# Kernel tuning notes

Hardware: AMD Instinct MI355X
Metric: run time of the kernel (lower is better)

The kernel has to match this reference:

```python
import jax, jax.numpy as jnp
import numpy as np

VOCAB = 32000
D_MODEL = 192
N_LAYERS = 8
D_STATE = 64
EXPAND = 2
D_CONV = 3
NUM_CLASSES = 2
D_INNER = EXPAND * D_MODEL            # 384
DT_RANK = (D_MODEL + 15) // 16        # 12 (mamba_ssm default ceil(d_model/16))
EPS = 1e-6


def rmsnorm(x, w):
    return w * x * jax.lax.rsqrt(jnp.mean(x * x, axis=-1, keepdims=True) + EPS)


def selective_scan(u, dt, A, Bm, Cm):
    # u, dt: (b, T, d_inner); Bm, Cm: (b, T, d_state); A: (d_inner, d_state)
    def step(h, xs):
        dt_t, B_t, C_t, u_t = xs                      # (b,di),(b,ds),(b,ds),(b,di)
        dA = jnp.exp(dt_t[:, :, None] * A)            # (b, di, ds)
        h = dA * h + (dt_t * u_t)[:, :, None] * B_t[:, None, :]
        y = jnp.einsum('bdn,bn->bd', h, C_t)
        return h, y

    b = u.shape[0]
    h0 = jnp.zeros((b, D_INNER, D_STATE), u.dtype)
    xs = (jnp.swapaxes(dt, 0, 1), jnp.swapaxes(Bm, 0, 1),
          jnp.swapaxes(Cm, 0, 1), jnp.swapaxes(u, 0, 1))
    _, ys = jax.lax.scan(step, h0, xs)                # ys: (T, b, di)
    return jnp.swapaxes(ys, 0, 1)


def mamba_layer(x, p):
    # one residual Mamba block: x + Mamba(RMSNorm(x))
    norm_w, in_w, cw, cb, xpw, dtw, dtb, Alog, Dp, ow = p
    h = rmsnorm(x, norm_w)
    xz = jnp.einsum('btd,ed->bte', h, in_w)           # (b, T, 2*di)
    xi, z = jnp.split(xz, 2, axis=-1)
    # causal depthwise conv over time
    xc = jnp.swapaxes(xi, 1, 2)                       # (b, di, T)
    xc = jax.lax.conv_general_dilated(xc, cw[:, None, :], (1,),
                                      [(D_CONV - 1, 0)],
                                      feature_group_count=D_INNER)
    xi = jax.nn.silu(jnp.swapaxes(xc, 1, 2) + cb)
    dbl = jnp.einsum('btc,ec->bte', xi, xpw)          # (b, T, dt_rank+2*ds)
    dt_r = dbl[..., :DT_RANK]
    Bm = dbl[..., DT_RANK:DT_RANK + D_STATE]
    Cm = dbl[..., DT_RANK + D_STATE:]
    dt = jax.nn.softplus(jnp.einsum('btr,dr->btd', dt_r, dtw) + dtb)
    A = -jnp.exp(Alog)
    y = selective_scan(xi, dt, A, Bm, Cm) + xi * Dp
    y = y * jax.nn.silu(z)
    return x + jnp.einsum('bte,de->btd', y, ow)


def setup_inputs():
    key = jax.random.key(0)
    ks = jax.random.split(key, 12)
    B, L = 8, 1024
    s = 0.02
    input_ids = jax.random.randint(ks[0], (B, L), 0, VOCAB, dtype=jnp.int32)
    attention_mask = jnp.ones((B, L), dtype=jnp.int32)
    embed = jax.random.normal(ks[1], (VOCAB, D_MODEL), jnp.float32) * s
    cls = jax.random.normal(ks[2], (1, 1, D_MODEL), jnp.float32) * s
    norm_w = jnp.ones((N_LAYERS, D_MODEL), jnp.float32)
    in_proj_w = jax.random.normal(ks[3], (N_LAYERS, 2 * D_INNER, D_MODEL), jnp.float32) * s
    conv_w = jax.random.normal(ks[4], (N_LAYERS, D_INNER, D_CONV), jnp.float32) * s
    conv_b = jnp.zeros((N_LAYERS, D_INNER), jnp.float32)
    x_proj_w = jax.random.normal(ks[5], (N_LAYERS, DT_RANK + 2 * D_STATE, D_INNER), jnp.float32) * s
    dt_proj_w = jax.random.normal(ks[6], (N_LAYERS, D_INNER, DT_RANK), jnp.float32) * s
    dt_proj_b = jnp.zeros((N_LAYERS, D_INNER), jnp.float32)
    # mamba_ssm S4D-real init: A_log = log(1..d_state)
    A_log = jnp.log(jnp.tile(jnp.arange(1.0, D_STATE + 1, dtype=jnp.float32)[None, None, :],
                             (N_LAYERS, D_INNER, 1)))
    D_param = jnp.ones((N_LAYERS, D_INNER), jnp.float32)
    out_proj_w = jax.random.normal(ks[7], (N_LAYERS, D_MODEL, D_INNER), jnp.float32) * s
    final_norm_w = jnp.ones((D_MODEL,), jnp.float32)
    head_w = embed[:NUM_CLASSES]            # tie_embeddings=True
    head_b = jnp.zeros((NUM_CLASSES,), jnp.float32)
    return dict(input_ids=input_ids, attention_mask=attention_mask, embed=embed,
                cls=cls, norm_w=norm_w, in_proj_w=in_proj_w, conv_w=conv_w,
                conv_b=conv_b, x_proj_w=x_proj_w, dt_proj_w=dt_proj_w,
                dt_proj_b=dt_proj_b, A_log=A_log, D_param=D_param,
                out_proj_w=out_proj_w, final_norm_w=final_norm_w,
                head_w=head_w, head_b=head_b)


def reference(input_ids, attention_mask, embed, cls, norm_w, in_proj_w, conv_w,
              conv_b, x_proj_w, dt_proj_w, dt_proj_b, A_log, D_param,
              out_proj_w, final_norm_w, head_w, head_b):
    x = embed[input_ids]                               # (b, L, d)
    b = x.shape[0]
    x = jnp.concatenate([x, jnp.broadcast_to(cls, (b, 1, D_MODEL))], axis=1)
    layer_fn = jax.checkpoint(mamba_layer)

    def body(x, p):
        return layer_fn(x, p), None

    x, _ = jax.lax.scan(body, x, (norm_w, in_proj_w, conv_w, conv_b, x_proj_w,
                                  dt_proj_w, dt_proj_b, A_log, D_param, out_proj_w))
    x = rmsnorm(x, final_norm_w)
    m = attention_mask.astype(x.dtype)                 # (b, L)
    denom = jnp.clip(jnp.sum(m, axis=1, keepdims=True), 1.0, None)
    pooled = jnp.sum(x[:, :-1] * m[..., None], axis=1) / denom
    return pooled @ head_w.T + head_b                  # (b, num_classes)
```

## Files before the change

### kernel.cpp

```cpp
#include <hip/hip_runtime.h>
#include <hip/hip_bf16.h>
#include <cstddef>

namespace {

constexpr int NB   = 8;
constexpr int LSEQ = 1025;
constexpr int TSEQ = 1024;
constexpr int DM   = 192;
constexpr int DI   = 384;
constexpr int DXZ  = 768;
constexpr int DBLW = 140;
constexpr int DTR  = 12;
constexpr int NST  = 64;
constexpr int MROWS = NB * LSEQ;
constexpr int NCH  = 64;
constexpr int CS   = 16;
constexpr int NCH1 = NCH - 1;
constexpr int NDG  = DI / 64;
constexpr int HST  = 32;
constexpr int XPAD = 144;
constexpr float LOG2E = 1.4426950408889634f;

using bf16x8 = __attribute__((ext_vector_type(8))) short;
using f32x4  = __attribute__((ext_vector_type(4))) float;

__device__ __forceinline__ float waveReduceSum(float v) {
#pragma unroll
  for (int o = 32; o; o >>= 1) v += __shfl_xor(v, o, 64);
  return v;
}

__device__ __forceinline__ unsigned short f2bf(float v) {
  __hip_bfloat16 b = __float2bfloat16(v);
  return *reinterpret_cast<unsigned short*>(&b);
}
__device__ __forceinline__ float bf2f(unsigned short u) {
  return __uint_as_float(((unsigned)u) << 16);
}
__device__ __forceinline__ unsigned addpair_bf(unsigned a, unsigned b) {
  float alo = __uint_as_float(a << 16), ahi = __uint_as_float(a & 0xffff0000u);
  float blo = __uint_as_float(b << 16), bhi = __uint_as_float(b & 0xffff0000u);
  return ((unsigned)f2bf(alo + blo)) | (((unsigned)f2bf(ahi + bhi)) << 16);
}

__global__ void embed_kernel(const int* __restrict__ ids, const float* __restrict__ emb,
                             const float* __restrict__ cls, float* __restrict__ x) {
  int idx = blockIdx.x * blockDim.x + threadIdx.x;
  if (idx >= NB * LSEQ * DM) return;
  int d = idx % DM;
  int bt = idx / DM;
  int t = bt % LSEQ, b = bt / LSEQ;
  float v;
  if (t < TSEQ) v = emb[(size_t)ids[b * TSEQ + t] * DM + d];
  else          v = cls[d];
  x[idx] = v;
}

__global__ void cvt_bf16_kernel(const float* __restrict__ src, unsigned short* __restrict__ dst,
                                int n) {
  int idx = blockIdx.x * blockDim.x + threadIdx.x;
  if (idx < n) dst[idx] = f2bf(src[idx]);
}

__global__ void pad_xp_kernel(const float* __restrict__ src, unsigned short* __restrict__ dst) {
  int idx = blockIdx.x * blockDim.x + threadIdx.x;
  if (idx >= 8 * XPAD * DI) return;
  int k = idx % DI;
  int n = (idx / DI) % XPAD;
  int l = idx / (DI * XPAD);
  float v = (n < DBLW) ? src[((size_t)l * DBLW + n) * DI + k] : 0.f;
  dst[idx] = f2bf(v);
}

__global__ void transpose_batched(const float* __restrict__ in, float* __restrict__ out,
                                  int rows, int cols) {
  __shared__ float tile[32][33];
  int l = blockIdx.z;
  int r0 = blockIdx.y * 32, c0 = blockIdx.x * 32;
  const float* src = in + (size_t)l * rows * cols;
  float* dst = out + (size_t)l * rows * cols;
  int tx = threadIdx.x, ty = threadIdx.y;
#pragma unroll
  for (int i = 0; i < 32; i += 8) {
    int r = r0 + ty + i, c = c0 + tx;
    if (r < rows && c < cols) tile[ty + i][tx] = src[(size_t)r * cols + c];
  }
  __syncthreads();
#pragma unroll
  for (int i = 0; i < 32; i += 8) {
    int c = c0 + ty + i, r = r0 + tx;
    if (c < cols && r < rows) dst[(size_t)c * rows + r] = tile[tx][ty + i];
  }
}

__global__ __launch_bounds__(192)
void rmsnorm_kernel(const float* __restrict__ x, const float* __restrict__ w,
                    unsigned short* __restrict__ h) {
  int row = blockIdx.x;
  int d = threadIdx.x;
  float v = x[(size_t)row * DM + d];
  float ss = waveReduceSum(v * v);
  __shared__ float red[3];
  if ((d & 63) == 0) red[d >> 6] = ss;
  __syncthreads();
  float ms = (red[0] + red[1] + red[2]) * (1.f / DM);
  h[(size_t)row * DM + d] = f2bf(v * rsqrtf(ms + 1e-6f) * w[d]);
}

template <int EPI, int ASRC>
__global__ __launch_bounds__(256)
void gemm_mfma(const unsigned short* __restrict__ A, const unsigned short* __restrict__ Ab0,
               const unsigned short* __restrict__ Ab1, const unsigned short* __restrict__ W,
               float* __restrict__ C, unsigned short* __restrict__ Cb,
               int M, int Nw, int Nstore, int K, int ldc) {
  __shared__ unsigned short Alds[128][40];
  __shared__ unsigned short Wlds[64][40];
  const int tid = threadIdx.x;
  const int w = tid >> 6, lane = tid & 63;
  const int r16 = lane & 15, g = lane >> 4;
  const int row0 = blockIdx.y * 128, col0 = blockIdx.x * 64;

  f32x4 acc[2][4];
#pragma unroll
  for (int mi = 0; mi < 2; ++mi)
#pragma unroll
    for (int ni = 0; ni < 4; ++ni) acc[mi][ni] = (f32x4){0.f, 0.f, 0.f, 0.f};

  for (int k0 = 0; k0 < K; k0 += 32) {
#pragma unroll
    for (int cc = 0; cc < 2; ++cc) {
      int c = tid + cc * 256;
      int r = c >> 2, q = c & 3;
      uint4 v = make_uint4(0, 0, 0, 0);
      int grow = row0 + r;
      if (grow < M) {
        if (ASRC == 0) {
          v = *(const uint4*)(A + (size_t)grow * K + k0 + q * 8);
        } else {
          uint4 a = *(const uint4*)(Ab0 + (size_t)grow * K + k0 + q * 8);
          uint4 b = *(const uint4*)(Ab1 + (size_t)grow * K + k0 + q * 8);
          v.x = addpair_bf(a.x, b.x);
          v.y = addpair_bf(a.y, b.y);
          v.z = addpair_bf(a.z, b.z);
          v.w = addpair_bf(a.w, b.w);
        }
      }
      *(uint4*)&Alds[r][q * 8] = v;
    }
    {
      int r = tid >> 2, q = tid & 3;
      uint4 v = make_uint4(0, 0, 0, 0);
      int gn = col0 + r;
      if (gn < Nw) v = *(const uint4*)(W + (size_t)gn * K + k0 + q * 8);
      *(uint4*)&Wlds[r][q * 8] = v;
    }
    __syncthreads();
    bf16x8 a_f[2], b_f[4];
#pragma unroll
    for (int mi = 0; mi < 2; ++mi)
      a_f[mi] = *(const bf16x8*)&Alds[w * 32 + mi * 16 + r16][g * 8];
#pragma unroll
    for (int ni = 0; ni < 4; ++ni)
      b_f[ni] = *(const bf16x8*)&Wlds[ni * 16 + r16][g * 8];
#pragma unroll
    for (int mi = 0; mi < 2; ++mi)
#pragma unroll
      for (int ni = 0; ni < 4; ++ni)
        acc[mi][ni] = __builtin_amdgcn_mfma_f32_16x16x32_bf16(a_f[mi], b_f[ni],
                                                              acc[mi][ni], 0, 0, 0);
    __syncthreads();
  }
#pragma unroll
  for (int mi = 0; mi < 2; ++mi) {
#pragma unroll
    for (int reg = 0; reg < 4; ++reg) {
      int row = row0 + w * 32 + mi * 16 + g * 4 + reg;
      if (row >= M) continue;
#pragma unroll
      for (int ni = 0; ni < 4; ++ni) {
        int col = col0 + ni * 16 + r16;
        if (col >= Nstore) continue;
        size_t idx = (size_t)row * ldc + col;
        if (EPI == 1)      C[idx] += acc[mi][ni][reg];
        else if (EPI == 0) C[idx] = acc[mi][ni][reg];
        else               Cb[idx] = f2bf(acc[mi][ni][reg]);
      }
    }
  }
}

__global__ void conv_kernel(const unsigned short* __restrict__ xz16, const float* __restrict__ cw,
                            const float* __restrict__ cb,
                            unsigned short* __restrict__ xi16,
                            unsigned short* __restrict__ zg16) {
  int idx = blockIdx.x * blockDim.x + threadIdx.x;
  if (idx >= NB * LSEQ * DI) return;
  int c = idx % DI;
  int bt = idx / DI;
  int t = bt % LSEQ, b = bt / LSEQ;
  const unsigned short* src = xz16 + (size_t)b * LSEQ * DXZ + c;
  float s = cb[c];
  float w0 = cw[c * 3 + 0], w1 = cw[c * 3 + 1], w2 = cw[c * 3 + 2];
  if (t >= 2) s = fmaf(w0, bf2f(src[(size_t)(t - 2) * DXZ]), s);
  if (t >= 1) s = fmaf(w1, bf2f(src[(size_t)(t - 1) * DXZ]), s);
  s = fmaf(w2, bf2f(src[(size_t)t * DXZ]), s);
  float sig = 1.f / (1.f + __expf(-s));
  float u = s * sig;
  xi16[idx] = f2bf(u);
  float zv = bf2f(src[(size_t)t * DXZ + DI]);
  float zsig = 1.f / (1.f + __expf(-zv));
  zg16[idx] = f2bf(zv * zsig);
}

__global__ __launch_bounds__(384)
void dt_kernel(const float* __restrict__ dbl, const float* __restrict__ dtwT,
               const float* __restrict__ dtb, float* __restrict__ dtout) {
  int row0 = blockIdx.x * 4;
  int d = threadIdx.x;
  __shared__ float rr[4][DTR];
  if (d < 4 * DTR) rr[d / DTR][d % DTR] = dbl[(size_t)(row0 + d / DTR) * DBLW + (d % DTR)];
  float w[DTR];
#pragma unroll
  for (int r = 0; r < DTR; ++r) w[r] = dtwT[r * DI + d];
  float bias = dtb[d];
  __syncthreads();
#pragma unroll
  for (int q = 0; q < 4; ++q) {
    float s = bias;
#pragma unroll
    for (int r = 0; r < DTR; ++r) s = fmaf(rr[q][r], w[r], s);
    float sp = fmaxf(s, 0.f) + log1pf(__expf(-fabsf(s)));
    dtout[(size_t)(row0 + q) * DI + d] = sp;
  }
}


__global__ __launch_bounds__(768, 6)
void scan_pass1(const float* __restrict__ dtp_, const unsigned short* __restrict__ xi16,
                const float* __restrict__ dbl, const float* __restrict__ Alog,
                float* __restrict__ cumdt, float* __restrict__ H) {
  __shared__ float Bt[CS][64];
  const int tid = threadIdx.x;
  const int w = tid >> 6, lane = tid & 63;
  const int dgrp = w >> 1, half = w & 1;
  const int b = blockIdx.x / NCH1;
  const int c = blockIdx.x % NCH1;
  const int bg = b * NDG + dgrp;
  const int d = dgrp * 64 + lane;
  const int n0 = half * HST;
  const int t0 = c * CS;

  {
    const float* srcB = dbl + ((size_t)b * LSEQ + t0) * DBLW + DTR + lane;
    for (int r = w; r < CS; r += 12) Bt[r][lane] = srcB[(size_t)r * DBLW];
  }

  const float* Ap = Alog + (size_t)d * NST;
  float a0 = __expf(Ap[0]);
  bool okl = true;
#pragma unroll
  for (int j = 0; j < HST; ++j) {
    float aj = __expf(Ap[n0 + j]);
    okl = okl && (fabsf(aj - (float)(n0 + j + 1) * a0) <= 1e-3f * (float)(n0 + j + 1) * fabsf(a0));
  }
  const bool fast = __all(okl);
  const float al2u = -a0 * LOG2E;

  float h[HST];
#pragma unroll
  for (int j = 0; j < HST; ++j) h[j] = 0.f;

  __syncthreads();

  const float* dtp = dtp_ + ((size_t)b * LSEQ + t0) * DI + d;
  const unsigned short* up = xi16 + ((size_t)b * LSEQ + t0) * DI + d;
  float cum = 0.f;
  float dtv = *dtp, uv = bf2f(*up);

  if (fast) {
    for (int t = 0; t < CS; ++t) {
      float n_dt = 0.f, n_u = 0.f;
      if (t + 1 < CS) {
        dtp += DI; up += DI;
        n_dt = *dtp; n_u = bf2f(*up);
      }
      float dtu = dtv * uv;
      float m = dtv * al2u;
      float r1 = exp2f(m);
      float p = (n0 == 0) ? r1 : exp2f(m * (float)(n0 + 1));
      float r2 = r1 * r1, r4 = r2 * r2;
      float s0 = p, s1 = p * r1, s2 = p * r2, s3 = s2 * r1;
#pragma unroll
      for (int k = 0; k < 8; ++k) {
        float4 B4 = *(const float4*)&Bt[t][n0 + 4 * k];
        h[4 * k + 0] = fmaf(s0, h[4 * k + 0], dtu * B4.x);
        h[4 * k + 1] = fmaf(s1, h[4 * k + 1], dtu * B4.y);
        h[4 * k + 2] = fmaf(s2, h[4 * k + 2], dtu * B4.z);
        h[4 * k + 3] = fmaf(s3, h[4 * k + 3], dtu * B4.w);
        if (k < 7) { s0 *= r4; s1 *= r4; s2 *= r4; s3 *= r4; }
      }
      cum += dtv;
      dtv = n_dt; uv = n_u;
    }
  } else {
    for (int t = 0; t < CS; ++t) {
      float n_dt = 0.f, n_u = 0.f;
      if (t + 1 < CS) {
        dtp += DI; up += DI;
        n_dt = *dtp; n_u = bf2f(*up);
      }
      float dtu = dtv * uv;
      for (int j = 0; j < HST; ++j) {
        float aj = -__expf(Ap[n0 + j]) * LOG2E;
        h[j] = fmaf(exp2f(dtv * aj), h[j], dtu * Bt[t][n0 + j]);
      }
      cum += dtv;
      dtv = n_dt; uv = n_u;
    }
  }

  if (half == 0)
    cumdt[(size_t)bg * NCH1 * 64 + (size_t)c * 64 + lane] = cum;
  float* hp = H + ((size_t)bg * NCH + (c + 1)) * NST * 64 + (size_t)n0 * 64 + lane;
#pragma unroll
  for (int j = 0; j < HST; ++j) hp[j * 64] = h[j];
}

__global__ __launch_bounds__(256)
void scan_pass2(const float* __restrict__ cumdt, const float* __restrict__ Alog,
                float* __restrict__ H) {
  int gw = blockIdx.x * 4 + (threadIdx.x >> 6);
  int lane = threadIdx.x & 63;
  int bg = gw >> 4;
  int nq = (gw & 15) * 4;
  int dgrp = bg % NDG;
  int d = dgrp * 64 + lane;

  float al2[4];
#pragma unroll
  for (int j = 0; j < 4; ++j) al2[j] = -__expf(Alog[(size_t)d * NST + nq + j]) * LOG2E;

  float h[4] = {0.f, 0.f, 0.f, 0.f};

  float* H0 = H + ((size_t)bg * NCH) * NST * 64 + (size_t)nq * 64 + lane;
#pragma unroll
  for (int j = 0; j < 4; ++j) H0[j * 64] = 0.f;

  for (int c = 1; c < NCH; ++c) {
    float cum = cumdt[(size_t)bg * NCH1 * 64 + (size_t)(c - 1) * 64 + lane];
    float* Hc = H + ((size_t)bg * NCH + c) * NST * 64 + (size_t)nq * 64 + lane;
#pragma unroll
    for (int j = 0; j < 4; ++j) {
      float he = Hc[j * 64];
      h[j] = fmaf(exp2f(al2[j] * cum), h[j], he);
      Hc[j * 64] = h[j];
    }
  }
}

__global__ __launch_bounds__(768, 6)
void scan_pass3(const float* __restrict__ dtp_, const unsigned short* __restrict__ xi16,
                const unsigned short* __restrict__ zg16, const float* __restrict__ dbl,
                const float* __restrict__ Alog, const float* __restrict__ Dpar,
                const float* __restrict__ H, unsigned short* __restrict__ yb0,
                unsigned short* __restrict__ yb1) {
  __shared__ float Bt[CS + 1][64];
  __shared__ float Ct[CS + 1][64];
  const int tid = threadIdx.x;
  const int w = tid >> 6, lane = tid & 63;
  const int dgrp = w >> 1, half = w & 1;
  const int b = blockIdx.x >> 6;
  const int c = blockIdx.x & 63;
  const int bg = b * NDG + dgrp;
  const int d = dgrp * 64 + lane;
  const int n0 = half * HST;
  const int t0 = c * CS;
  const int nsteps = (c == NCH - 1) ? (LSEQ - t0) : CS;

  {
    if (w < 6) {
      const float* srcB = dbl + ((size_t)b * LSEQ + t0) * DBLW + DTR + lane;
      for (int r = w; r < nsteps; r += 6) Bt[r][lane] = srcB[(size_t)r * DBLW];
    } else {
      const float* srcC = dbl + ((size_t)b * LSEQ + t0) * DBLW + DTR + NST + lane;
      for (int r = w - 6; r < nsteps; r += 6) Ct[r][lane] = srcC[(size_t)r * DBLW];
    }
  }

  const float* Ap = Alog + (size_t)d * NST;
  float a0 = __expf(Ap[0]);
  bool okl = true;
#pragma unroll
  for (int j = 0; j < HST; ++j) {
    float aj = __expf(Ap[n0 + j]);
    okl = okl && (fabsf(aj - (float)(n0 + j + 1) * a0) <= 1e-3f * (float)(n0 + j + 1) * fabsf(a0));
  }
  const bool fast = __all(okl);
  const float al2u = -a0 * LOG2E;

  float Dp = Dpar[d];
  float h[HST];
  {
    const float* hi = H + ((size_t)bg * NCH + c) * NST * 64 + (size_t)n0 * 64 + lane;
#pragma unroll
    for (int j = 0; j < HST; ++j) h[j] = hi[j * 64];
  }

  __syncthreads();

  const float* dtp = dtp_ + ((size_t)b * LSEQ + t0) * DI + d;
  const unsigned short* up = xi16 + ((size_t)b * LSEQ + t0) * DI + d;
  const unsigned short* gp = zg16 + ((size_t)b * LSEQ + t0) * DI + d;
  unsigned short* yp = (half == 0 ? yb0 : yb1) + ((size_t)b * LSEQ + t0) * DI + d;

  float dtv = *dtp, uv = bf2f(*up), gv = bf2f(*gp);

  if (fast) {
    for (int t = 0; t < nsteps; ++t) {
      float n_dt = 0.f, n_u = 0.f, n_g = 0.f;
      if (t + 1 < nsteps) {
        dtp += DI; up += DI; gp += DI;
        n_dt = *dtp; n_u = bf2f(*up); n_g = bf2f(*gp);
      }
      float dtu = dtv * uv;
      float m = dtv * al2u;
      float r1 = exp2f(m);
      float p = (n0 == 0) ? r1 : exp2f(m * (float)(n0 + 1));
      float r2 = r1 * r1, r4 = r2 * r2;
      float s0 = p, s1 = p * r1, s2 = p * r2, s3 = s2 * r1;
      float y = 0.f;
#pragma unroll
      for (int k = 0; k < 8; ++k) {
        float4 B4 = *(const float4*)&Bt[t][n0 + 4 * k];
        float4 C4 = *(const float4*)&Ct[t][n0 + 4 * k];
        h[4 * k + 0] = fmaf(s0, h[4 * k + 0], dtu * B4.x);
        y = fmaf(h[4 * k + 0], C4.x, y);
        h[4 * k + 1] = fmaf(s1, h[4 * k + 1], dtu * B4.y);
        y = fmaf(h[4 * k + 1], C4.y, y);
        h[4 * k + 2] = fmaf(s2, h[4 * k + 2], dtu * B4.z);
        y = fmaf(h[4 * k + 2], C4.z, y);
        h[4 * k + 3] = fmaf(s3, h[4 * k + 3], dtu * B4.w);
        y = fmaf(h[4 * k + 3], C4.w, y);
        if (k < 7) { s0 *= r4; s1 *= r4; s2 *= r4; s3 *= r4; }
      }
      float outv = (half == 0) ? fmaf(uv, Dp, y) * gv : y * gv;
      *yp = f2bf(outv);
      yp += DI;
      dtv = n_dt; uv = n_u; gv = n_g;
    }
  } else {
    for (int t = 0; t < nsteps; ++t) {
      float n_dt = 0.f, n_u = 0.f, n_g = 0.f;
      if (t + 1 < nsteps) {
        dtp += DI; up += DI; gp += DI;
        n_dt = *dtp; n_u = bf2f(*up); n_g = bf2f(*gp);
      }
      float dtu = dtv * uv;
      float y = 0.f;
      for (int j = 0; j < HST; ++j) {
        float aj = -__expf(Ap[n0 + j]) * LOG2E;
        h[j] = fmaf(exp2f(dtv * aj), h[j], dtu * Bt[t][n0 + j]);
        y = fmaf(h[j], Ct[t][n0 + j], y);
      }
      float outv = (half == 0) ? fmaf(uv, Dp, y) * gv : y * gv;
      *yp = f2bf(outv);
      yp += DI;
      dtv = n_dt; uv = n_u; gv = n_g;
    }
  }
}

__global__ __launch_bounds__(192)
void pool1_kernel(const float* __restrict__ x, const int* __restrict__ mask,
                  const float* __restrict__ fw, float* __restrict__ partial) {
  int b = blockIdx.x >> 6;
  int chunk = blockIdx.x & 63;
  int d = threadIdx.x;
  __shared__ float red[3];
  float w = fw[d];
  float acc = 0.f;
  for (int tt = 0; tt < 16; ++tt) {
    int t = chunk * 16 + tt;
    float v = x[((size_t)b * LSEQ + t) * DM + d];
    float ss = waveReduceSum(v * v);
    if ((d & 63) == 0) red[d >> 6] = ss;
    __syncthreads();
    float ms = (red[0] + red[1] + red[2]) * (1.f / DM);
    float m = (float)mask[b * TSEQ + t];
    acc = fmaf(v * rsqrtf(ms + 1e-6f) * w, m, acc);
    __syncthreads();
  }
  partial[((size_t)b * 64 + chunk) * DM + d] = acc;
}

__global__ __launch_bounds__(192)
void pool2_kernel(const float* __restrict__ partial, const int* __restrict__ mask,
                  const float* __restrict__ hw, const float* __restrict__ hb,
                  float* __restrict__ out) {
  int b = blockIdx.x;
  int d = threadIdx.x;
  float s = 0.f;
  for (int c = 0; c < 64; ++c) s += partial[((size_t)b * 64 + c) * DM + d];
  float den = 0.f;
  for (int t = d; t < TSEQ; t += DM) den += (float)mask[b * TSEQ + t];
  den = waveReduceSum(den);
  __shared__ float dred[3];
  __shared__ float pooled[DM];
  if ((d & 63) == 0) dred[d >> 6] = den;
  __syncthreads();
  float denom = fmaxf(dred[0] + dred[1] + dred[2], 1.f);
  pooled[d] = s / denom;
  __syncthreads();
  if (d < 2) {
    float acc = hb[d];
    for (int k = 0; k < DM; ++k) acc = fmaf(pooled[k], hw[d * DM + k], acc);
    out[b * 2 + d] = acc;
  }
}

}

extern "C" void kernel_launch(void* const* d_in, const int* in_sizes, int n_in,
                              void* d_out, int out_size, void* d_ws, size_t ws_size,
                              hipStream_t stream) {
  const int*   ids    = (const int*)d_in[0];
  const int*   mask   = (const int*)d_in[1];
  const float* embed  = (const float*)d_in[2];
  const float* cls    = (const float*)d_in[3];
  const float* norm_w = (const float*)d_in[4];
  const float* in_w   = (const float*)d_in[5];
  const float* conv_w = (const float*)d_in[6];
  const float* conv_b = (const float*)d_in[7];
  const float* xp_w   = (const float*)d_in[8];
  const float* dtw    = (const float*)d_in[9];
  const float* dtb    = (const float*)d_in[10];
  const float* Alog   = (const float*)d_in[11];
  const float* Dpar   = (const float*)d_in[12];
  const float* ow     = (const float*)d_in[13];
  const float* fnw    = (const float*)d_in[14];
  const float* hw     = (const float*)d_in[15];
  const float* hb     = (const float*)d_in[16];
  float* out = (float*)d_out;

  char* base = (char*)d_ws;
  size_t off = 0;
  auto alloc = [&](size_t bytes) -> void* {
    void* p = base + off;
    off = (off + bytes + 255) & ~(size_t)255;
    return p;
  };

  float* x      = (float*)alloc((size_t)NB * LSEQ * DM * 4);
  unsigned short* h16 = (unsigned short*)alloc((size_t)NB * LSEQ * DM * 2);
  unsigned short* xz16 = (unsigned short*)alloc((size_t)NB * LSEQ * DXZ * 2);
  unsigned short* xi16 = (unsigned short*)alloc((size_t)NB * LSEQ * DI * 2);
  unsigned short* zg16 = (unsigned short*)alloc((size_t)NB * LSEQ * DI * 2);
  float* dblb   = (float*)alloc((size_t)NB * LSEQ * DBLW * 4);
  float* dtbuf  = (float*)alloc((size_t)NB * LSEQ * DI * 4);
  unsigned short* yb0 = (unsigned short*)alloc((size_t)NB * LSEQ * DI * 2);
  unsigned short* yb1 = (unsigned short*)alloc((size_t)NB * LSEQ * DI * 2);
  unsigned short* wb_in = (unsigned short*)alloc((size_t)8 * DXZ * DM * 2);
  unsigned short* wb_xp = (unsigned short*)alloc((size_t)8 * XPAD * DI * 2);
  unsigned short* wb_ow = (unsigned short*)alloc((size_t)8 * DM * DI * 2);
  float* wT_dt  = (float*)alloc((size_t)8 * DTR * DI * 4);
  float* partial = (float*)alloc((size_t)NB * 64 * DM * 4);
  float* cumdt  = (float*)alloc((size_t)NB * NDG * NCH1 * 64 * 4);
  float* Hbuf   = (float*)alloc((size_t)NB * NDG * NCH * NST * 64 * 4);

  cvt_bf16_kernel<<<(8 * DXZ * DM + 255) / 256, 256, 0, stream>>>(in_w, wb_in, 8 * DXZ * DM);
  pad_xp_kernel<<<(8 * XPAD * DI + 255) / 256, 256, 0, stream>>>(xp_w, wb_xp);
  cvt_bf16_kernel<<<(8 * DM * DI + 255) / 256, 256, 0, stream>>>(ow, wb_ow, 8 * DM * DI);
  dim3 tb(32, 8);
  transpose_batched<<<dim3(1, 12, 8), tb, 0, stream>>>(dtw, wT_dt, DI, DTR);

  embed_kernel<<<(NB * LSEQ * DM) / 256, 256, 0, stream>>>(ids, embed, cls, x);

  const int mtiles = (MROWS + 127) / 128;
  for (int l = 0; l < 8; ++l) {
    rmsnorm_kernel<<<MROWS, 192, 0, stream>>>(x, norm_w + l * DM, h16);
    gemm_mfma<2, 0><<<dim3(DXZ / 64, mtiles), 256, 0, stream>>>(
        h16, nullptr, nullptr, wb_in + (size_t)l * DXZ * DM, nullptr, xz16,
        MROWS, DXZ, DXZ, DM, DXZ);
    conv_kernel<<<(NB * LSEQ * DI) / 256, 256, 0, stream>>>(
        xz16, conv_w + l * DI * 3, conv_b + l * DI, xi16, zg16);
    gemm_mfma<0, 0><<<dim3(XPAD / 64 + 1, mtiles), 256, 0, stream>>>(
        xi16, nullptr, nullptr, wb_xp + (size_t)l * XPAD * DI, dblb, nullptr,
        MROWS, XPAD, DBLW, DI, DBLW);
    dt_kernel<<<MROWS / 4, DI, 0, stream>>>(dblb, wT_dt + l * DTR * DI, dtb + l * DI, dtbuf);
    scan_pass1<<<NB * NCH1, 768, 0, stream>>>(
        dtbuf, xi16, dblb, Alog + (size_t)l * DI * NST, cumdt, Hbuf);
    scan_pass2<<<(NB * NDG * 16) / 4, 256, 0, stream>>>(
        cumdt, Alog + (size_t)l * DI * NST, Hbuf);
    scan_pass3<<<NB * NCH, 768, 0, stream>>>(
        dtbuf, xi16, zg16, dblb, Alog + (size_t)l * DI * NST, Dpar + l * DI, Hbuf,
        yb0, yb1);
    gemm_mfma<1, 1><<<dim3(DM / 64, mtiles), 256, 0, stream>>>(
        nullptr, yb0, yb1, wb_ow + (size_t)l * DM * DI, x, nullptr,
        MROWS, DM, DM, DI, DM);
  }

  pool1_kernel<<<NB * 64, 192, 0, stream>>>(x, mask, fnw, partial);
  pool2_kernel<<<NB, 192, 0, stream>>>(partial, mask, hw, hb, out);
}
```

Measured before the change: 1.391 ms.

## Store x_proj output and chunk states in bf16, use larger scan chunks

The x_proj GEMM now writes bf16 instead of fp32, and the dt and scan kernels read B/C from bf16 in shared memory as packed uint4 words. Inter-chunk state buffers H become bf16, and the chunk count drops from 64 to 32 with 32 steps per chunk, so there is half as much state traffic and a shorter sequential pass2. Pass3 also splits its y reduction into four independent accumulators to shorten the FMA dependency chain, and the launch-bounds occupancy hint drops from 6 to 3. In exchange, B, C, dt_r and the carried states lose precision, and there is less parallelism across chunks.

```diff
diff --git a/kernel.cpp b/kernel.cpp
--- a/kernel.cpp
+++ b/kernel.cpp
@@ -14,8 +14,8 @@
 constexpr int DTR  = 12;
 constexpr int NST  = 64;
 constexpr int MROWS = NB * LSEQ;
-constexpr int NCH  = 64;
-constexpr int CS   = 16;
+constexpr int NCH  = 32;
+constexpr int CS   = 32;
 constexpr int NCH1 = NCH - 1;
 constexpr int NDG  = DI / 64;
 constexpr int HST  = 32;
@@ -38,9 +38,11 @@
 __device__ __forceinline__ float bf2f(unsigned short u) {
   return __uint_as_float(((unsigned)u) << 16);
 }
+__device__ __forceinline__ float lo16(unsigned v) { return __uint_as_float(v << 16); }
+__device__ __forceinline__ float hi16(unsigned v) { return __uint_as_float(v & 0xffff0000u); }
 __device__ __forceinline__ unsigned addpair_bf(unsigned a, unsigned b) {
-  float alo = __uint_as_float(a << 16), ahi = __uint_as_float(a & 0xffff0000u);
-  float blo = __uint_as_float(b << 16), bhi = __uint_as_float(b & 0xffff0000u);
+  float alo = lo16(a), ahi = hi16(a);
+  float blo = lo16(b), bhi = hi16(b);
   return ((unsigned)f2bf(alo + blo)) | (((unsigned)f2bf(ahi + bhi)) << 16);
 }
 
@@ -214,12 +216,12 @@
 }
 
 __global__ __launch_bounds__(384)
-void dt_kernel(const float* __restrict__ dbl, const float* __restrict__ dtwT,
+void dt_kernel(const unsigned short* __restrict__ dbl16, const float* __restrict__ dtwT,
                const float* __restrict__ dtb, float* __restrict__ dtout) {
   int row0 = blockIdx.x * 4;
   int d = threadIdx.x;
   __shared__ float rr[4][DTR];
-  if (d < 4 * DTR) rr[d / DTR][d % DTR] = dbl[(size_t)(row0 + d / DTR) * DBLW + (d % DTR)];
+  if (d < 4 * DTR) rr[d / DTR][d % DTR] = bf2f(dbl16[(size_t)(row0 + d / DTR) * DBLW + (d % DTR)]);
   float w[DTR];
 #pragma unroll
   for (int r = 0; r < DTR; ++r) w[r] = dtwT[r * DI + d];
@@ -236,11 +238,11 @@
 }
 
 
-__global__ __launch_bounds__(768, 6)
+__global__ __launch_bounds__(768, 3)
 void scan_pass1(const float* __restrict__ dtp_, const unsigned short* __restrict__ xi16,
-                const float* __restrict__ dbl, const float* __restrict__ Alog,
-                float* __restrict__ cumdt, float* __restrict__ H) {
-  __shared__ float Bt[CS][64];
+                const unsigned short* __restrict__ dbl16, const float* __restrict__ Alog,
+                float* __restrict__ cumdt, unsigned short* __restrict__ H) {
+  __shared__ unsigned short Bt16[CS][64];
   const int tid = threadIdx.x;
   const int w = tid >> 6, lane = tid & 63;
   const int dgrp = w >> 1, half = w & 1;
@@ -252,8 +254,8 @@
   const int t0 = c * CS;
 
   {
-    const float* srcB = dbl + ((size_t)b * LSEQ + t0) * DBLW + DTR + lane;
-    for (int r = w; r < CS; r += 12) Bt[r][lane] = srcB[(size_t)r * DBLW];
+    const unsigned short* srcB = dbl16 + ((size_t)b * LSEQ + t0) * DBLW + DTR + lane;
+    for (int r = w; r < CS; r += 12) Bt16[r][lane] = srcB[(size_t)r * DBLW];
   }
 
   const float* Ap = Alog + (size_t)d * NST;
@@ -291,14 +293,21 @@
       float p = (n0 == 0) ? r1 : exp2f(m * (float)(n0 + 1));
       float r2 = r1 * r1, r4 = r2 * r2;
       float s0 = p, s1 = p * r1, s2 = p * r2, s3 = s2 * r1;
-#pragma unroll
-      for (int k = 0; k < 8; ++k) {
-        float4 B4 = *(const float4*)&Bt[t][n0 + 4 * k];
-        h[4 * k + 0] = fmaf(s0, h[4 * k + 0], dtu * B4.x);
-        h[4 * k + 1] = fmaf(s1, h[4 * k + 1], dtu * B4.y);
-        h[4 * k + 2] = fmaf(s2, h[4 * k + 2], dtu * B4.z);
-        h[4 * k + 3] = fmaf(s3, h[4 * k + 3], dtu * B4.w);
-        if (k < 7) { s0 *= r4; s1 *= r4; s2 *= r4; s3 *= r4; }
+      const uint4* Bq = (const uint4*)&Bt16[t][n0];
+#pragma unroll
+      for (int q = 0; q < 4; ++q) {
+        uint4 bq = Bq[q];
+        int j = 8 * q;
+        h[j + 0] = fmaf(s0, h[j + 0], dtu * lo16(bq.x));
+        h[j + 1] = fmaf(s1, h[j + 1], dtu * hi16(bq.x));
+        h[j + 2] = fmaf(s2, h[j + 2], dtu * lo16(bq.y));
+        h[j + 3] = fmaf(s3, h[j + 3], dtu * hi16(bq.y));
+        s0 *= r4; s1 *= r4; s2 *= r4; s3 *= r4;
+        h[j + 4] = fmaf(s0, h[j + 4], dtu * lo16(bq.z));
+        h[j + 5] = fmaf(s1, h[j + 5], dtu * hi16(bq.z));
+        h[j + 6] = fmaf(s2, h[j + 6], dtu * lo16(bq.w));
+        h[j + 7] = fmaf(s3, h[j + 7], dtu * hi16(bq.w));
+        if (q < 3) { s0 *= r4; s1 *= r4; s2 *= r4; s3 *= r4; }
       }
       cum += dtv;
       dtv = n_dt; uv = n_u;
@@ -313,7 +322,7 @@
       float dtu = dtv * uv;
       for (int j = 0; j < HST; ++j) {
         float aj = -__expf(Ap[n0 + j]) * LOG2E;
-        h[j] = fmaf(exp2f(dtv * aj), h[j], dtu * Bt[t][n0 + j]);
+        h[j] = fmaf(exp2f(dtv * aj), h[j], dtu * bf2f(Bt16[t][n0 + j]));
       }
       cum += dtv;
       dtv = n_dt; uv = n_u;
@@ -322,14 +331,14 @@
 
   if (half == 0)
     cumdt[(size_t)bg * NCH1 * 64 + (size_t)c * 64 + lane] = cum;
-  float* hp = H + ((size_t)bg * NCH + (c + 1)) * NST * 64 + (size_t)n0 * 64 + lane;
-#pragma unroll
-  for (int j = 0; j < HST; ++j) hp[j * 64] = h[j];
+  unsigned short* hp = H + ((size_t)bg * NCH + (c + 1)) * NST * 64 + (size_t)n0 * 64 + lane;
+#pragma unroll
+  for (int j = 0; j < HST; ++j) hp[j * 64] = f2bf(h[j]);
 }
 
 __global__ __launch_bounds__(256)
 void scan_pass2(const float* __restrict__ cumdt, const float* __restrict__ Alog,
-                float* __restrict__ H) {
+                unsigned short* __restrict__ H) {
   int gw = blockIdx.x * 4 + (threadIdx.x >> 6);
   int lane = threadIdx.x & 63;
   int bg = gw >> 4;
@@ -343,35 +352,35 @@
 
   float h[4] = {0.f, 0.f, 0.f, 0.f};
 
-  float* H0 = H + ((size_t)bg * NCH) * NST * 64 + (size_t)nq * 64 + lane;
-#pragma unroll
-  for (int j = 0; j < 4; ++j) H0[j * 64] = 0.f;
+  unsigned short* H0 = H + ((size_t)bg * NCH) * NST * 64 + (size_t)nq * 64 + lane;
+#pragma unroll
+  for (int j = 0; j < 4; ++j) H0[j * 64] = 0;
 
   for (int c = 1; c < NCH; ++c) {
     float cum = cumdt[(size_t)bg * NCH1 * 64 + (size_t)(c - 1) * 64 + lane];
-    float* Hc = H + ((size_t)bg * NCH + c) * NST * 64 + (size_t)nq * 64 + lane;
+    unsigned short* Hc = H + ((size_t)bg * NCH + c) * NST * 64 + (size_t)nq * 64 + lane;
 #pragma unroll
     for (int j = 0; j < 4; ++j) {
-      float he = Hc[j * 64];
+      float he = bf2f(Hc[j * 64]);
       h[j] = fmaf(exp2f(al2[j] * cum), h[j], he);
-      Hc[j * 64] = h[j];
-    }
-  }
-}
-
-__global__ __launch_bounds__(768, 6)
+      Hc[j * 64] = f2bf(h[j]);
+    }
+  }
+}
+
+__global__ __launch_bounds__(768, 3)
 void scan_pass3(const float* __restrict__ dtp_, const unsigned short* __restrict__ xi16,
-                const unsigned short* __restrict__ zg16, const float* __restrict__ dbl,
+                const unsigned short* __restrict__ zg16, const unsigned short* __restrict__ dbl16,
                 const float* __restrict__ Alog, const float* __restrict__ Dpar,
-                const float* __restrict__ H, unsigned short* __restrict__ yb0,
+                const unsigned short* __restrict__ H, unsigned short* __restrict__ yb0,
                 unsigned short* __restrict__ yb1) {
-  __shared__ float Bt[CS + 1][64];
-  __shared__ float Ct[CS + 1][64];
+  __shared__ unsigned short Bt16[CS + 1][64];
+  __shared__ unsigned short Ct16[CS + 1][64];
   const int tid = threadIdx.x;
   const int w = tid >> 6, lane = tid & 63;
   const int dgrp = w >> 1, half = w & 1;
-  const int b = blockIdx.x >> 6;
-  const int c = blockIdx.x & 63;
+  const int b = blockIdx.x >> 5;
+  const int c = blockIdx.x & 31;
   const int bg = b * NDG + dgrp;
   const int d = dgrp * 64 + lane;
   const int n0 = half * HST;
@@ -380,11 +389,11 @@
 
   {
     if (w < 6) {
-      const float* srcB = dbl + ((size_t)b * LSEQ + t0) * DBLW + DTR + lane;
-      for (int r = w; r < nsteps; r += 6) Bt[r][lane] = srcB[(size_t)r * DBLW];
+      const unsigned short* srcB = dbl16 + ((size_t)b * LSEQ + t0) * DBLW + DTR + lane;
+      for (int r = w; r < nsteps; r += 6) Bt16[r][lane] = srcB[(size_t)r * DBLW];
     } else {
-      const float* srcC = dbl + ((size_t)b * LSEQ + t0) * DBLW + DTR + NST + lane;
-      for (int r = w - 6; r < nsteps; r += 6) Ct[r][lane] = srcC[(size_t)r * DBLW];
+      const unsigned short* srcC = dbl16 + ((size_t)b * LSEQ + t0) * DBLW + DTR + NST + lane;
+      for (int r = w - 6; r < nsteps; r += 6) Ct16[r][lane] = srcC[(size_t)r * DBLW];
     }
   }
 
@@ -402,9 +411,9 @@
   float Dp = Dpar[d];
   float h[HST];
   {
-    const float* hi = H + ((size_t)bg * NCH + c) * NST * 64 + (size_t)n0 * 64 + lane;
-#pragma unroll
-    for (int j = 0; j < HST; ++j) h[j] = hi[j * 64];
+    const unsigned short* hi = H + ((size_t)bg * NCH + c) * NST * 64 + (size_t)n0 * 64 + lane;
+#pragma unroll
+    for (int j = 0; j < HST; ++j) h[j] = bf2f(hi[j * 64]);
   }
 
   __syncthreads();
@@ -429,21 +438,34 @@
       float p = (n0 == 0) ? r1 : exp2f(m * (float)(n0 + 1));
       float r2 = r1 * r1, r4 = r2 * r2;
       float s0 = p, s1 = p * r1, s2 = p * r2, s3 = s2 * r1;
-      float y = 0.f;
-#pragma unroll
-      for (int k = 0; k < 8; ++k) {
-        float4 B4 = *(const float4*)&Bt[t][n0 + 4 * k];
-        float4 C4 = *(const float4*)&Ct[t][n0 + 4 * k];
-        h[4 * k + 0] = fmaf(s0, h[4 * k + 0], dtu * B4.x);
-        y = fmaf(h[4 * k + 0], C4.x, y);
-        h[4 * k + 1] = fmaf(s1, h[4 * k + 1], dtu * B4.y);
-        y = fmaf(h[4 * k + 1], C4.y, y);
-        h[4 * k + 2] = fmaf(s2, h[4 * k + 2], dtu * B4.z);
-        y = fmaf(h[4 * k + 2], C4.z, y);
-        h[4 * k + 3] = fmaf(s3, h[4 * k + 3], dtu * B4.w);
-        y = fmaf(h[4 * k + 3], C4.w, y);
-        if (k < 7) { s0 *= r4; s1 *= r4; s2 *= r4; s3 *= r4; }
-      }
+      float y0 = 0.f, y1 = 0.f, y2 = 0.f, y3 = 0.f;
+      const uint4* Bq = (const uint4*)&Bt16[t][n0];
+      const uint4* Cq = (const uint4*)&Ct16[t][n0];
+#pragma unroll
+      for (int q = 0; q < 4; ++q) {
+        uint4 bq = Bq[q];
+        uint4 cq = Cq[q];
+        int j = 8 * q;
+        h[j + 0] = fmaf(s0, h[j + 0], dtu * lo16(bq.x));
+        y0 = fmaf(h[j + 0], lo16(cq.x), y0);
+        h[j + 1] = fmaf(s1, h[j + 1], dtu * hi16(bq.x));
+        y1 = fmaf(h[j + 1], hi16(cq.x), y1);
+        h[j + 2] = fmaf(s2, h[j + 2], dtu * lo16(bq.y));
+        y2 = fmaf(h[j + 2], lo16(cq.y), y2);
+        h[j + 3] = fmaf(s3, h[j + 3], dtu * hi16(bq.y));
+        y3 = fmaf(h[j + 3], hi16(cq.y), y3);
+        s0 *= r4; s1 *= r4; s2 *= r4; s3 *= r4;
+        h[j + 4] = fmaf(s0, h[j + 4], dtu * lo16(bq.z));
+        y0 = fmaf(h[j + 4], lo16(cq.z), y0);
+        h[j + 5] = fmaf(s1, h[j + 5], dtu * hi16(bq.z));
+        y1 = fmaf(h[j + 5], hi16(cq.z), y1);
+        h[j + 6] = fmaf(s2, h[j + 6], dtu * lo16(bq.w));
+        y2 = fmaf(h[j + 6], lo16(cq.w), y2);
+        h[j + 7] = fmaf(s3, h[j + 7], dtu * hi16(bq.w));
+        y3 = fmaf(h[j + 7], hi16(cq.w), y3);
+        if (q < 3) { s0 *= r4; s1 *= r4; s2 *= r4; s3 *= r4; }
+      }
+      float y = (y0 + y1) + (y2 + y3);
       float outv = (half == 0) ? fmaf(uv, Dp, y) * gv : y * gv;
       *yp = f2bf(outv);
       yp += DI;
@@ -460,8 +482,8 @@
       float y = 0.f;
       for (int j = 0; j < HST; ++j) {
         float aj = -__expf(Ap[n0 + j]) * LOG2E;
-        h[j] = fmaf(exp2f(dtv * aj), h[j], dtu * Bt[t][n0 + j]);
-        y = fmaf(h[j], Ct[t][n0 + j], y);
+        h[j] = fmaf(exp2f(dtv * aj), h[j], dtu * bf2f(Bt16[t][n0 + j]));
+        y = fmaf(h[j], bf2f(Ct16[t][n0 + j]), y);
       }
       float outv = (half == 0) ? fmaf(uv, Dp, y) * gv : y * gv;
       *yp = f2bf(outv);
@@ -556,7 +578,7 @@
   unsigned short* xz16 = (unsigned short*)alloc((size_t)NB * LSEQ * DXZ * 2);
   unsigned short* xi16 = (unsigned short*)alloc((size_t)NB * LSEQ * DI * 2);
   unsigned short* zg16 = (unsigned short*)alloc((size_t)NB * LSEQ * DI * 2);
-  float* dblb   = (float*)alloc((size_t)NB * LSEQ * DBLW * 4);
+  unsigned short* dblb16 = (unsigned short*)alloc((size_t)NB * LSEQ * DBLW * 2);
   float* dtbuf  = (float*)alloc((size_t)NB * LSEQ * DI * 4);
   unsigned short* yb0 = (unsigned short*)alloc((size_t)NB * LSEQ * DI * 2);
   unsigned short* yb1 = (unsigned short*)alloc((size_t)NB * LSEQ * DI * 2);
@@ -566,7 +588,7 @@
   float* wT_dt  = (float*)alloc((size_t)8 * DTR * DI * 4);
   float* partial = (float*)alloc((size_t)NB * 64 * DM * 4);
   float* cumdt  = (float*)alloc((size_t)NB * NDG * NCH1 * 64 * 4);
-  float* Hbuf   = (float*)alloc((size_t)NB * NDG * NCH * NST * 64 * 4);
+  unsigned short* Hbuf = (unsigned short*)alloc((size_t)NB * NDG * NCH * NST * 64 * 2);
 
   cvt_bf16_kernel<<<(8 * DXZ * DM + 255) / 256, 256, 0, stream>>>(in_w, wb_in, 8 * DXZ * DM);
   pad_xp_kernel<<<(8 * XPAD * DI + 255) / 256, 256, 0, stream>>>(xp_w, wb_xp);
@@ -584,16 +606,16 @@
         MROWS, DXZ, DXZ, DM, DXZ);
     conv_kernel<<<(NB * LSEQ * DI) / 256, 256, 0, stream>>>(
         xz16, conv_w + l * DI * 3, conv_b + l * DI, xi16, zg16);
-    gemm_mfma<0, 0><<<dim3(XPAD / 64 + 1, mtiles), 256, 0, stream>>>(
-        xi16, nullptr, nullptr, wb_xp + (size_t)l * XPAD * DI, dblb, nullptr,
+    gemm_mfma<2, 0><<<dim3(XPAD / 64 + 1, mtiles), 256, 0, stream>>>(
+        xi16, nullptr, nullptr, wb_xp + (size_t)l * XPAD * DI, nullptr, dblb16,
         MROWS, XPAD, DBLW, DI, DBLW);
-    dt_kernel<<<MROWS / 4, DI, 0, stream>>>(dblb, wT_dt + l * DTR * DI, dtb + l * DI, dtbuf);
+    dt_kernel<<<MROWS / 4, DI, 0, stream>>>(dblb16, wT_dt + l * DTR * DI, dtb + l * DI, dtbuf);
     scan_pass1<<<NB * NCH1, 768, 0, stream>>>(
-        dtbuf, xi16, dblb, Alog + (size_t)l * DI * NST, cumdt, Hbuf);
+        dtbuf, xi16, dblb16, Alog + (size_t)l * DI * NST, cumdt, Hbuf);
     scan_pass2<<<(NB * NDG * 16) / 4, 256, 0, stream>>>(
         cumdt, Alog + (size_t)l * DI * NST, Hbuf);
     scan_pass3<<<NB * NCH, 768, 0, stream>>>(
-        dtbuf, xi16, zg16, dblb, Alog + (size_t)l * DI * NST, Dpar + l * DI, Hbuf,
+        dtbuf, xi16, zg16, dblb16, Alog + (size_t)l * DI * NST, Dpar + l * DI, Hbuf,
         yb0, yb1);
     gemm_mfma<1, 1><<<dim3(DM / 64, mtiles), 256, 0, stream>>>(
         nullptr, yb0, yb1, wb_ow + (size_t)l * DM * DI, x, nullptr,
```

Result: no change. 1.364 ms (-1.9%).

## Restructure chunked scan: larger chunks, bf16 carry states, fused z-gate into pass3

Applied to the files above, without the earlier changes.

Doubles the scan chunk length and halves the chunk count, and splits each batch-chunk into two blocks of 384 threads that each cover half the channel groups. Inter-chunk carry states are stored in bf16 instead of fp32, halving that traffic. The silu(z) gate is no longer precomputed by the conv kernel; pass3 reads z from xz16 and computes the gate inline, which removes the zg16 buffer write and read. Pass3 also splits its y accumulation into four partial sums for more ILP. The risks are precision loss from bf16 carries, a longer serial scan per chunk, and strided reads of z.

```diff
diff --git a/kernel.cpp b/kernel.cpp
--- a/kernel.cpp
+++ b/kernel.cpp
@@ -14,8 +14,8 @@
 constexpr int DTR  = 12;
 constexpr int NST  = 64;
 constexpr int MROWS = NB * LSEQ;
-constexpr int NCH  = 64;
-constexpr int CS   = 16;
+constexpr int NCH  = 32;
+constexpr int CS   = 32;
 constexpr int NCH1 = NCH - 1;
 constexpr int NDG  = DI / 64;
 constexpr int HST  = 32;
@@ -38,9 +38,11 @@
 __device__ __forceinline__ float bf2f(unsigned short u) {
   return __uint_as_float(((unsigned)u) << 16);
 }
+__device__ __forceinline__ float lo16(unsigned v) { return __uint_as_float(v << 16); }
+__device__ __forceinline__ float hi16(unsigned v) { return __uint_as_float(v & 0xffff0000u); }
 __device__ __forceinline__ unsigned addpair_bf(unsigned a, unsigned b) {
-  float alo = __uint_as_float(a << 16), ahi = __uint_as_float(a & 0xffff0000u);
-  float blo = __uint_as_float(b << 16), bhi = __uint_as_float(b & 0xffff0000u);
+  float alo = lo16(a), ahi = hi16(a);
+  float blo = lo16(b), bhi = hi16(b);
   return ((unsigned)f2bf(alo + blo)) | (((unsigned)f2bf(ahi + bhi)) << 16);
 }
 
@@ -192,8 +194,7 @@
 
 __global__ void conv_kernel(const unsigned short* __restrict__ xz16, const float* __restrict__ cw,
                             const float* __restrict__ cb,
-                            unsigned short* __restrict__ xi16,
-                            unsigned short* __restrict__ zg16) {
+                            unsigned short* __restrict__ xi16) {
   int idx = blockIdx.x * blockDim.x + threadIdx.x;
   if (idx >= NB * LSEQ * DI) return;
   int c = idx % DI;
@@ -206,11 +207,7 @@
   if (t >= 1) s = fmaf(w1, bf2f(src[(size_t)(t - 1) * DXZ]), s);
   s = fmaf(w2, bf2f(src[(size_t)t * DXZ]), s);
   float sig = 1.f / (1.f + __expf(-s));
-  float u = s * sig;
-  xi16[idx] = f2bf(u);
-  float zv = bf2f(src[(size_t)t * DXZ + DI]);
-  float zsig = 1.f / (1.f + __expf(-zv));
-  zg16[idx] = f2bf(zv * zsig);
+  xi16[idx] = f2bf(s * sig);
 }
 
 __global__ __launch_bounds__(384)
@@ -236,16 +233,18 @@
 }
 
 
-__global__ __launch_bounds__(768, 6)
+__global__ __launch_bounds__(384, 5)
 void scan_pass1(const float* __restrict__ dtp_, const unsigned short* __restrict__ xi16,
                 const float* __restrict__ dbl, const float* __restrict__ Alog,
-                float* __restrict__ cumdt, float* __restrict__ H) {
+                float* __restrict__ cumdt, unsigned short* __restrict__ H) {
   __shared__ float Bt[CS][64];
   const int tid = threadIdx.x;
   const int w = tid >> 6, lane = tid & 63;
-  const int dgrp = w >> 1, half = w & 1;
-  const int b = blockIdx.x / NCH1;
-  const int c = blockIdx.x % NCH1;
+  const int dgrp_l = w >> 1, half = w & 1;
+  const int b = blockIdx.x / (NCH1 * 2);
+  const int rem = blockIdx.x % (NCH1 * 2);
+  const int c = rem >> 1, dh = rem & 1;
+  const int dgrp = dh * 3 + dgrp_l;
   const int bg = b * NDG + dgrp;
   const int d = dgrp * 64 + lane;
   const int n0 = half * HST;
@@ -253,7 +252,7 @@
 
   {
     const float* srcB = dbl + ((size_t)b * LSEQ + t0) * DBLW + DTR + lane;
-    for (int r = w; r < CS; r += 12) Bt[r][lane] = srcB[(size_t)r * DBLW];
+    for (int r = w; r < CS; r += 6) Bt[r][lane] = srcB[(size_t)r * DBLW];
   }
 
   const float* Ap = Alog + (size_t)d * NST;
@@ -322,14 +321,14 @@
 
   if (half == 0)
     cumdt[(size_t)bg * NCH1 * 64 + (size_t)c * 64 + lane] = cum;
-  float* hp = H + ((size_t)bg * NCH + (c + 1)) * NST * 64 + (size_t)n0 * 64 + lane;
-#pragma unroll
-  for (int j = 0; j < HST; ++j) hp[j * 64] = h[j];
+  unsigned short* hp = H + ((size_t)bg * NCH + (c + 1)) * NST * 64 + (size_t)n0 * 64 + lane;
+#pragma unroll
+  for (int j = 0; j < HST; ++j) hp[j * 64] = f2bf(h[j]);
 }
 
 __global__ __launch_bounds__(256)
 void scan_pass2(const float* __restrict__ cumdt, const float* __restrict__ Alog,
-                float* __restrict__ H) {
+                unsigned short* __restrict__ H) {
   int gw = blockIdx.x * 4 + (threadIdx.x >> 6);
   int lane = threadIdx.x & 63;
   int bg = gw >> 4;
@@ -343,35 +342,37 @@
 
   float h[4] = {0.f, 0.f, 0.f, 0.f};
 
-  float* H0 = H + ((size_t)bg * NCH) * NST * 64 + (size_t)nq * 64 + lane;
-#pragma unroll
-  for (int j = 0; j < 4; ++j) H0[j * 64] = 0.f;
+  unsigned short* H0 = H + ((size_t)bg * NCH) * NST * 64 + (size_t)nq * 64 + lane;
+#pragma unroll
+  for (int j = 0; j < 4; ++j) H0[j * 64] = 0;
 
   for (int c = 1; c < NCH; ++c) {
     float cum = cumdt[(size_t)bg * NCH1 * 64 + (size_t)(c - 1) * 64 + lane];
-    float* Hc = H + ((size_t)bg * NCH + c) * NST * 64 + (size_t)nq * 64 + lane;
+    unsigned short* Hc = H + ((size_t)bg * NCH + c) * NST * 64 + (size_t)nq * 64 + lane;
 #pragma unroll
     for (int j = 0; j < 4; ++j) {
-      float he = Hc[j * 64];
+      float he = bf2f(Hc[j * 64]);
       h[j] = fmaf(exp2f(al2[j] * cum), h[j], he);
-      Hc[j * 64] = h[j];
-    }
-  }
-}
-
-__global__ __launch_bounds__(768, 6)
+      Hc[j * 64] = f2bf(h[j]);
+    }
+  }
+}
+
+__global__ __launch_bounds__(384, 5)
 void scan_pass3(const float* __restrict__ dtp_, const unsigned short* __restrict__ xi16,
-                const unsigned short* __restrict__ zg16, const float* __restrict__ dbl,
+                const unsigned short* __restrict__ xz16, const float* __restrict__ dbl,
                 const float* __restrict__ Alog, const float* __restrict__ Dpar,
-                const float* __restrict__ H, unsigned short* __restrict__ yb0,
+                const unsigned short* __restrict__ H, unsigned short* __restrict__ yb0,
                 unsigned short* __restrict__ yb1) {
   __shared__ float Bt[CS + 1][64];
   __shared__ float Ct[CS + 1][64];
   const int tid = threadIdx.x;
   const int w = tid >> 6, lane = tid & 63;
-  const int dgrp = w >> 1, half = w & 1;
-  const int b = blockIdx.x >> 6;
-  const int c = blockIdx.x & 63;
+  const int dgrp_l = w >> 1, half = w & 1;
+  const int b = blockIdx.x / (NCH * 2);
+  const int rem = blockIdx.x % (NCH * 2);
+  const int c = rem >> 1, dh = rem & 1;
+  const int dgrp = dh * 3 + dgrp_l;
   const int bg = b * NDG + dgrp;
   const int d = dgrp * 64 + lane;
   const int n0 = half * HST;
@@ -379,12 +380,12 @@
   const int nsteps = (c == NCH - 1) ? (LSEQ - t0) : CS;
 
   {
-    if (w < 6) {
+    if (w < 3) {
       const float* srcB = dbl + ((size_t)b * LSEQ + t0) * DBLW + DTR + lane;
-      for (int r = w; r < nsteps; r += 6) Bt[r][lane] = srcB[(size_t)r * DBLW];
+      for (int r = w; r < nsteps; r += 3) Bt[r][lane] = srcB[(size_t)r * DBLW];
     } else {
       const float* srcC = dbl + ((size_t)b * LSEQ + t0) * DBLW + DTR + NST + lane;
-      for (int r = w - 6; r < nsteps; r += 6) Ct[r][lane] = srcC[(size_t)r * DBLW];
+      for (int r = w - 3; r < nsteps; r += 3) Ct[r][lane] = srcC[(size_t)r * DBLW];
     }
   }
 
@@ -402,26 +403,26 @@
   float Dp = Dpar[d];
   float h[HST];
   {
-    const float* hi = H + ((size_t)bg * NCH + c) * NST * 64 + (size_t)n0 * 64 + lane;
-#pragma unroll
-    for (int j = 0; j < HST; ++j) h[j] = hi[j * 64];
+    const unsigned short* hi = H + ((size_t)bg * NCH + c) * NST * 64 + (size_t)n0 * 64 + lane;
+#pragma unroll
+    for (int j = 0; j < HST; ++j) h[j] = bf2f(hi[j * 64]);
   }
 
   __syncthreads();
 
   const float* dtp = dtp_ + ((size_t)b * LSEQ + t0) * DI + d;
   const unsigned short* up = xi16 + ((size_t)b * LSEQ + t0) * DI + d;
-  const unsigned short* gp = zg16 + ((size_t)b * LSEQ + t0) * DI + d;
+  const unsigned short* zp = xz16 + ((size_t)b * LSEQ + t0) * DXZ + DI + d;
   unsigned short* yp = (half == 0 ? yb0 : yb1) + ((size_t)b * LSEQ + t0) * DI + d;
 
-  float dtv = *dtp, uv = bf2f(*up), gv = bf2f(*gp);
+  float dtv = *dtp, uv = bf2f(*up), zv = bf2f(*zp);
 
   if (fast) {
     for (int t = 0; t < nsteps; ++t) {
-      float n_dt = 0.f, n_u = 0.f, n_g = 0.f;
+      float n_dt = 0.f, n_u = 0.f, n_z = 0.f;
       if (t + 1 < nsteps) {
-        dtp += DI; up += DI; gp += DI;
-        n_dt = *dtp; n_u = bf2f(*up); n_g = bf2f(*gp);
+        dtp += DI; up += DI; zp += DXZ;
+        n_dt = *dtp; n_u = bf2f(*up); n_z = bf2f(*zp);
       }
       float dtu = dtv * uv;
       float m = dtv * al2u;
@@ -429,32 +430,34 @@
       float p = (n0 == 0) ? r1 : exp2f(m * (float)(n0 + 1));
       float r2 = r1 * r1, r4 = r2 * r2;
       float s0 = p, s1 = p * r1, s2 = p * r2, s3 = s2 * r1;
-      float y = 0.f;
+      float y0 = 0.f, y1 = 0.f, y2 = 0.f, y3 = 0.f;
 #pragma unroll
       for (int k = 0; k < 8; ++k) {
         float4 B4 = *(const float4*)&Bt[t][n0 + 4 * k];
         float4 C4 = *(const float4*)&Ct[t][n0 + 4 * k];
         h[4 * k + 0] = fmaf(s0, h[4 * k + 0], dtu * B4.x);
-        y = fmaf(h[4 * k + 0], C4.x, y);
+        y0 = fmaf(h[4 * k + 0], C4.x, y0);
         h[4 * k + 1] = fmaf(s1, h[4 * k + 1], dtu * B4.y);
-        y = fmaf(h[4 * k + 1], C4.y, y);
+        y1 = fmaf(h[4 * k + 1], C4.y, y1);
         h[4 * k + 2] = fmaf(s2, h[4 * k + 2], dtu * B4.z);
-        y = fmaf(h[4 * k + 2], C4.z, y);
+        y2 = fmaf(h[4 * k + 2], C4.z, y2);
         h[4 * k + 3] = fmaf(s3, h[4 * k + 3], dtu * B4.w);
-        y = fmaf(h[4 * k + 3], C4.w, y);
+        y3 = fmaf(h[4 * k + 3], C4.w, y3);
         if (k < 7) { s0 *= r4; s1 *= r4; s2 *= r4; s3 *= r4; }
       }
+      float y = (y0 + y1) + (y2 + y3);
+      float gv = zv / (1.f + __expf(-zv));
       float outv = (half == 0) ? fmaf(uv, Dp, y) * gv : y * gv;
       *yp = f2bf(outv);
       yp += DI;
-      dtv = n_dt; uv = n_u; gv = n_g;
+      dtv = n_dt; uv = n_u; zv = n_z;
     }
   } else {
     for (int t = 0; t < nsteps; ++t) {
-      float n_dt = 0.f, n_u = 0.f, n_g = 0.f;
+      float n_dt = 0.f, n_u = 0.f, n_z = 0.f;
       if (t + 1 < nsteps) {
-        dtp += DI; up += DI; gp += DI;
-        n_dt = *dtp; n_u = bf2f(*up); n_g = bf2f(*gp);
+        dtp += DI; up += DI; zp += DXZ;
+        n_dt = *dtp; n_u = bf2f(*up); n_z = bf2f(*zp);
       }
       float dtu = dtv * uv;
       float y = 0.f;
@@ -463,10 +466,11 @@
         h[j] = fmaf(exp2f(dtv * aj), h[j], dtu * Bt[t][n0 + j]);
         y = fmaf(h[j], Ct[t][n0 + j], y);
       }
+      float gv = zv / (1.f + __expf(-zv));
       float outv = (half == 0) ? fmaf(uv, Dp, y) * gv : y * gv;
       *yp = f2bf(outv);
       yp += DI;
-      dtv = n_dt; uv = n_u; gv = n_g;
+      dtv = n_dt; uv = n_u; zv = n_z;
     }
   }
 }
@@ -555,7 +559,6 @@
   unsigned short* h16 = (unsigned short*)alloc((size_t)NB * LSEQ * DM * 2);
   unsigned short* xz16 = (unsigned short*)alloc((size_t)NB * LSEQ * DXZ * 2);
   unsigned short* xi16 = (unsigned short*)alloc((size_t)NB * LSEQ * DI * 2);
-  unsigned short* zg16 = (unsigned short*)alloc((size_t)NB * LSEQ * DI * 2);
   float* dblb   = (float*)alloc((size_t)NB * LSEQ * DBLW * 4);
   float* dtbuf  = (float*)alloc((size_t)NB * LSEQ * DI * 4);
   unsigned short* yb0 = (unsigned short*)alloc((size_t)NB * LSEQ * DI * 2);
@@ -566,7 +569,7 @@
   float* wT_dt  = (float*)alloc((size_t)8 * DTR * DI * 4);
   float* partial = (float*)alloc((size_t)NB * 64 * DM * 4);
   float* cumdt  = (float*)alloc((size_t)NB * NDG * NCH1 * 64 * 4);
-  float* Hbuf   = (float*)alloc((size_t)NB * NDG * NCH * NST * 64 * 4);
+  unsigned short* Hbuf = (unsigned short*)alloc((size_t)NB * NDG * NCH * NST * 64 * 2);
 
   cvt_bf16_kernel<<<(8 * DXZ * DM + 255) / 256, 256, 0, stream>>>(in_w, wb_in, 8 * DXZ * DM);
   pad_xp_kernel<<<(8 * XPAD * DI + 255) / 256, 256, 0, stream>>>(xp_w, wb_xp);
@@ -583,17 +586,17 @@
         h16, nullptr, nullptr, wb_in + (size_t)l * DXZ * DM, nullptr, xz16,
         MROWS, DXZ, DXZ, DM, DXZ);
     conv_kernel<<<(NB * LSEQ * DI) / 256, 256, 0, stream>>>(
-        xz16, conv_w + l * DI * 3, conv_b + l * DI, xi16, zg16);
+        xz16, conv_w + l * DI * 3, conv_b + l * DI, xi16);
     gemm_mfma<0, 0><<<dim3(XPAD / 64 + 1, mtiles), 256, 0, stream>>>(
         xi16, nullptr, nullptr, wb_xp + (size_t)l * XPAD * DI, dblb, nullptr,
         MROWS, XPAD, DBLW, DI, DBLW);
     dt_kernel<<<MROWS / 4, DI, 0, stream>>>(dblb, wT_dt + l * DTR * DI, dtb + l * DI, dtbuf);
-    scan_pass1<<<NB * NCH1, 768, 0, stream>>>(
+    scan_pass1<<<NB * NCH1 * 2, 384, 0, stream>>>(
         dtbuf, xi16, dblb, Alog + (size_t)l * DI * NST, cumdt, Hbuf);
     scan_pass2<<<(NB * NDG * 16) / 4, 256, 0, stream>>>(
         cumdt, Alog + (size_t)l * DI * NST, Hbuf);
-    scan_pass3<<<NB * NCH, 768, 0, stream>>>(
-        dtbuf, xi16, zg16, dblb, Alog + (size_t)l * DI * NST, Dpar + l * DI, Hbuf,
+    scan_pass3<<<NB * NCH * 2, 384, 0, stream>>>(
+        dtbuf, xi16, xz16, dblb, Alog + (size_t)l * DI * NST, Dpar + l * DI, Hbuf,
         yb0, yb1);
     gemm_mfma<1, 1><<<dim3(DM / 64, mtiles), 256, 0, stream>>>(
         nullptr, yb0, yb1, wb_ow + (size_t)l * DM * DI, x, nullptr,
```

Result: slower. 1.518 ms (+9.1%).
